# Performance work log

Hardware: AMD Instinct MI355X
Metric: run time of the kernel (lower is better)

The kernel has to match this reference:

```python
import jax, jax.numpy as jnp
import numpy as np

D_HEAD = 128
WINDOW = 512
SCALE = D_HEAD ** -0.5

def setup_inputs() -> dict:
    key = jax.random.key(0)
    kq, kk, kv = jax.random.split(key, 3)
    shape = (4, 16, 2048, D_HEAD)  # [B, H, T, d_head]
    q = jax.random.normal(kq, shape, dtype=jnp.float32)
    k = jax.random.normal(kk, shape, dtype=jnp.float32)
    v = jax.random.normal(kv, shape, dtype=jnp.float32)
    return {"q": q, "k": k, "v": v}

def reference(q, k, v):
    # Sliding-window causal attention (BaseAttention._sliding_window_attention).
    T = q.shape[2]
    scores = jnp.einsum('bhqd,bhkd->bhqk', q, k) * SCALE  # [B,H,T,T]
    i = jnp.arange(T)
    causal = i[None, :] <= i[:, None]                      # j <= i
    in_window = (i[:, None] - i[None, :]) < WINDOW         # i - j < window
    mask = causal & in_window
    scores = jnp.where(mask, scores, -jnp.inf)
    attn = jax.nn.softmax(scores.astype(jnp.float32), axis=-1).astype(v.dtype)
    return jnp.einsum('bhqk,bhkd->bhqd', attn, v)
```

## Files before the change

### kernel.cpp

```cpp
#include <hip/hip_runtime.h>

#define T_SEQ   2048
#define DH      128
#define WINDOW  512
#define BM      128
#define BN      64
#define NT      32
#define TILE_US 16384
#define SCALE_F 0.08838834764831845f

typedef unsigned short ushort_t;
typedef __attribute__((ext_vector_type(8))) unsigned short ushort8;
typedef __attribute__((ext_vector_type(4))) unsigned short ushort4v;
typedef __attribute__((ext_vector_type(4))) float float4v;
typedef __attribute__((ext_vector_type(8))) __bf16 bf16x8;

union U8 { ushort8 us; bf16x8 bf; };

__device__ __forceinline__ unsigned short f2bf(float f) {
  union { float f; unsigned u; } x; x.f = f;
  unsigned r = x.u + 0x7FFFu + ((x.u >> 16) & 1u);
  return (unsigned short)(r >> 16);
}

__device__ __forceinline__ void async16(const ushort_t* g, ushort_t* l) {
  __builtin_amdgcn_global_load_lds(
      (const __attribute__((address_space(1))) unsigned int*)g,
      (__attribute__((address_space(3))) unsigned int*)l, 16, 0, 0);
}

__global__ __launch_bounds__(256)
void pack_kv(const float* __restrict__ kg, const float* __restrict__ vg,
             ushort_t* __restrict__ ws)
{
  const int tile = blockIdx.x;
  const int tid  = threadIdx.x;
  const size_t src = (size_t)tile * (BN * DH);
  const float* kb = kg + src;
  const float* vb = vg + src;
  ushort_t* wk = ws + (size_t)tile * TILE_US;
  ushort_t* wv = wk + 8192;

#pragma unroll
  for (int rep = 0; rep < 4; ++rep) {
    const int b   = rep * 256 + tid;
    const int key = b >> 4;
    const int c8  = b & 15;
    const float* s = kb + key * DH + c8 * 8;
    float4v a = *(const float4v*)s;
    float4v c = *(const float4v*)(s + 4);
    ushort8 h;
    h[0]=f2bf(a[0]); h[1]=f2bf(a[1]); h[2]=f2bf(a[2]); h[3]=f2bf(a[3]);
    h[4]=f2bf(c[0]); h[5]=f2bf(c[1]); h[6]=f2bf(c[2]); h[7]=f2bf(c[3]);
    *(ushort8*)(wk + key * DH + ((c8 ^ (key & 7)) << 3)) = h;
  }

  const int cb  = tid >> 3;
  const int rb0 = tid & 7;
#pragma unroll
  for (int it = 0; it < 2; ++it) {
    const int rb = rb0 + it * 8;
    const float* s = vb + (size_t)(rb * 4) * DH + cb * 4;
    float4v r0 = *(const float4v*)(s);
    float4v r1 = *(const float4v*)(s + DH);
    float4v r2 = *(const float4v*)(s + 2 * DH);
    float4v r3 = *(const float4v*)(s + 3 * DH);
#pragma unroll
    for (int c = 0; c < 4; ++c) {
      const int d = cb * 4 + c;
      ushort4v h;
      h[0]=f2bf(r0[c]); h[1]=f2bf(r1[c]); h[2]=f2bf(r2[c]); h[3]=f2bf(r3[c]);
      *(ushort4v*)(wv + d * BN + (((rb >> 1) ^ (d & 7)) << 3) + (rb & 1) * 4) = h;
    }
  }
}

#define PP 72

__global__ __launch_bounds__(512)
void swa_fwd(const float* __restrict__ qg, const ushort_t* __restrict__ ws,
             float* __restrict__ og)
{
  __shared__ ushort_t lds[TILE_US + 8 * 16 * PP];
  ushort_t* ldsK  = lds;
  ushort_t* ldsVt = lds + 8192;
  ushort_t* ldsP  = lds + TILE_US;

  const int qt   = blockIdx.x;
  const int bh   = blockIdx.y;
  const int tid  = threadIdx.x;
  const int wv   = tid >> 6;
  const int lane = tid & 63;
  const int quad = lane >> 4;
  const int ln16 = lane & 15;
  const int l7   = ln16 & 7;

  const size_t base = (size_t)bh * (T_SEQ * DH);
  const float* qb = qg + base;
  float*       ob = og + base;
  const ushort_t* wsb = ws + (size_t)bh * NT * TILE_US;

  const int i0w = qt * BM + wv * 16;

  bf16x8 qf[4];
  {
    const float* qrow = qb + (size_t)(i0w + ln16) * DH + quad * 8;
#pragma unroll
    for (int ks = 0; ks < 4; ++ks) {
      float4v a = *(const float4v*)(qrow + ks * 32);
      float4v b = *(const float4v*)(qrow + ks * 32 + 4);
      U8 u;
      u.us[0]=f2bf(a[0]*SCALE_F); u.us[1]=f2bf(a[1]*SCALE_F);
      u.us[2]=f2bf(a[2]*SCALE_F); u.us[3]=f2bf(a[3]*SCALE_F);
      u.us[4]=f2bf(b[0]*SCALE_F); u.us[5]=f2bf(b[1]*SCALE_F);
      u.us[6]=f2bf(b[2]*SCALE_F); u.us[7]=f2bf(b[3]*SCALE_F);
      qf[ks] = u.bf;
    }
  }

  float4v Oacc[8];
#pragma unroll
  for (int n = 0; n < 8; ++n) Oacc[n] = (float4v)(0.0f);
  float m_i[4] = {-1e30f, -1e30f, -1e30f, -1e30f};
  float l_i[4] = {0.f, 0.f, 0.f, 0.f};

  const int lo  = qt * BM - (WINDOW - 1);
  const int kt0 = (lo > 0) ? (lo >> 6) : 0;
  const int kt1 = (qt * BM + BM - 1) >> 6;

  for (int kt = kt0; kt <= kt1; ++kt) {
    {
      const ushort_t* wt = wsb + (size_t)kt * TILE_US;
#pragma unroll
      for (int rd = 0; rd < 4; ++rd) {
        const int off = (rd * 512 + tid) * 8;
        async16(wt + off, lds + off);
      }
    }
    __syncthreads();

    const int j0 = kt * BN;
    const bool wave_active = (j0 <= i0w + 15) && (i0w - j0 - 63 < WINDOW);
    if (wave_active) {
      float4v sv[4];
#pragma unroll
      for (int nt = 0; nt < 4; ++nt) {
        float4v acc = (float4v)(0.0f);
        const ushort_t* kp = ldsK + (nt * 16 + ln16) * DH;
#pragma unroll
        for (int ks = 0; ks < 4; ++ks) {
          U8 b; b.us = *(const ushort8*)(kp + (((ks * 4 + quad) ^ l7) << 3));
          acc = __builtin_amdgcn_mfma_f32_16x16x32_bf16(qf[ks], b.bf, acc, 0, 0, 0);
        }
        sv[nt] = acc;
      }

      const bool need_mask = (j0 + 63 > i0w) || ((i0w + 15) - j0 >= WINDOW);
      if (need_mask) {
#pragma unroll
        for (int nt = 0; nt < 4; ++nt) {
          const int j = j0 + nt * 16 + ln16;
#pragma unroll
          for (int r = 0; r < 4; ++r) {
            const int i = i0w + quad * 4 + r;
            const bool ok = (j <= i) && ((i - j) < WINDOW);
            sv[nt][r] = ok ? sv[nt][r] : -1e30f;
          }
        }
      }

      float alpha[4];
#pragma unroll
      for (int r = 0; r < 4; ++r) {
        float mt = fmaxf(fmaxf(sv[0][r], sv[1][r]), fmaxf(sv[2][r], sv[3][r]));
        mt = fmaxf(mt, __shfl_xor(mt, 1));
        mt = fmaxf(mt, __shfl_xor(mt, 2));
        mt = fmaxf(mt, __shfl_xor(mt, 4));
        mt = fmaxf(mt, __shfl_xor(mt, 8));
        const float mn = fmaxf(m_i[r], mt);
        alpha[r] = __expf(m_i[r] - mn);
        m_i[r] = mn;
      }

      ushort_t* pb = ldsP + wv * (16 * PP);
#pragma unroll
      for (int r = 0; r < 4; ++r) {
        float ps = 0.f;
#pragma unroll
        for (int nt = 0; nt < 4; ++nt) {
          const float p = __expf(sv[nt][r] - m_i[r]);
          ps += p;
          pb[(quad * 4 + r) * PP + nt * 16 + ln16] = f2bf(p);
        }
        l_i[r] = l_i[r] * alpha[r] + ps;
#pragma unroll
        for (int n = 0; n < 8; ++n) Oacc[n][r] *= alpha[r];
      }

#pragma unroll
      for (int ks = 0; ks < 2; ++ks) {
        U8 a; a.us = *(const ushort8*)(pb + ln16 * PP + ks * 32 + quad * 8);
#pragma unroll
        for (int n = 0; n < 8; ++n) {
          const ushort_t* vp = ldsVt + (n * 16 + ln16) * BN;
          U8 b; b.us = *(const ushort8*)(vp + (((ks * 4 + quad) ^ l7) << 3));
          Oacc[n] = __builtin_amdgcn_mfma_f32_16x16x32_bf16(a.bf, b.bf, Oacc[n], 0, 0, 0);
        }
      }
    }
    __syncthreads();
  }

  float linv[4];
#pragma unroll
  for (int r = 0; r < 4; ++r) {
    float s = l_i[r];
    s += __shfl_xor(s, 1);
    s += __shfl_xor(s, 2);
    s += __shfl_xor(s, 4);
    s += __shfl_xor(s, 8);
    linv[r] = 1.0f / s;
  }
  float* orow = ob + (size_t)(i0w + quad * 4) * DH + ln16;
#pragma unroll
  for (int r = 0; r < 4; ++r) {
#pragma unroll
    for (int n = 0; n < 8; ++n) {
      orow[(size_t)r * DH + n * 16] = Oacc[n][r] * linv[r];
    }
  }
}

extern "C" void kernel_launch(void* const* d_in, const int* in_sizes, int n_in,
                              void* d_out, int out_size, void* d_ws, size_t ws_size,
                              hipStream_t stream) {
  const float* q = (const float*)d_in[0];
  const float* k = (const float*)d_in[1];
  const float* v = (const float*)d_in[2];
  float* o = (float*)d_out;
  const int bh_count = in_sizes[0] / (T_SEQ * DH);
  ushort_t* ws = (ushort_t*)d_ws;

  pack_kv<<<dim3(bh_count * NT), 256, 0, stream>>>(k, v, ws);
  swa_fwd<<<dim3(T_SEQ / BM, bh_count), 512, 0, stream>>>(q, ws, o);
}
```

Measured before the change: 283.2 us.

## Switch attention to 32x32 MFMA with transposed scores and register-resident P

```diff
diff --git a/kernel.cpp b/kernel.cpp
--- a/kernel.cpp
+++ b/kernel.cpp
@@ -7,18 +7,20 @@
 #define BN      64
 #define NT      32
 #define TILE_US 16384
-#define SCALE_F 0.08838834764831845f
+#define SCALE_LOG2E 0.12751744250f
 
 typedef unsigned short ushort_t;
 typedef __attribute__((ext_vector_type(8))) unsigned short ushort8;
 typedef __attribute__((ext_vector_type(4))) unsigned short ushort4v;
 typedef __attribute__((ext_vector_type(4))) float float4v;
+typedef __attribute__((ext_vector_type(16))) float float16v;
 typedef __attribute__((ext_vector_type(8))) __bf16 bf16x8;
 
-union U8 { ushort8 us; bf16x8 bf; };
+union U8 { ushort8 us; bf16x8 bf; unsigned u[4]; };
+union FU { float f; unsigned u; };
 
 __device__ __forceinline__ unsigned short f2bf(float f) {
-  union { float f; unsigned u; } x; x.f = f;
+  FU x; x.f = f;
   unsigned r = x.u + 0x7FFFu + ((x.u >> 16) & 1u);
   return (unsigned short)(r >> 16);
 }
@@ -33,13 +35,12 @@
 void pack_kv(const float* __restrict__ kg, const float* __restrict__ vg,
              ushort_t* __restrict__ ws)
 {
+  __shared__ __align__(16) ushort_t sb[TILE_US];
   const int tile = blockIdx.x;
   const int tid  = threadIdx.x;
   const size_t src = (size_t)tile * (BN * DH);
   const float* kb = kg + src;
   const float* vb = vg + src;
-  ushort_t* wk = ws + (size_t)tile * TILE_US;
-  ushort_t* wv = wk + 8192;
 
 #pragma unroll
   for (int rep = 0; rep < 4; ++rep) {
@@ -49,184 +50,190 @@
     const float* s = kb + key * DH + c8 * 8;
     float4v a = *(const float4v*)s;
     float4v c = *(const float4v*)(s + 4);
-    ushort8 h;
-    h[0]=f2bf(a[0]); h[1]=f2bf(a[1]); h[2]=f2bf(a[2]); h[3]=f2bf(a[3]);
-    h[4]=f2bf(c[0]); h[5]=f2bf(c[1]); h[6]=f2bf(c[2]); h[7]=f2bf(c[3]);
-    *(ushort8*)(wk + key * DH + ((c8 ^ (key & 7)) << 3)) = h;
-  }
-
-  const int cb  = tid >> 3;
-  const int rb0 = tid & 7;
-#pragma unroll
-  for (int it = 0; it < 2; ++it) {
-    const int rb = rb0 + it * 8;
-    const float* s = vb + (size_t)(rb * 4) * DH + cb * 4;
-    float4v r0 = *(const float4v*)(s);
-    float4v r1 = *(const float4v*)(s + DH);
-    float4v r2 = *(const float4v*)(s + 2 * DH);
-    float4v r3 = *(const float4v*)(s + 3 * DH);
-#pragma unroll
-    for (int c = 0; c < 4; ++c) {
-      const int d = cb * 4 + c;
-      ushort4v h;
-      h[0]=f2bf(r0[c]); h[1]=f2bf(r1[c]); h[2]=f2bf(r2[c]); h[3]=f2bf(r3[c]);
-      *(ushort4v*)(wv + d * BN + (((rb >> 1) ^ (d & 7)) << 3) + (rb & 1) * 4) = h;
-    }
-  }
-}
-
-#define PP 72
-
-__global__ __launch_bounds__(512)
+    U8 h;
+    h.us[0]=f2bf(a[0]); h.us[1]=f2bf(a[1]); h.us[2]=f2bf(a[2]); h.us[3]=f2bf(a[3]);
+    h.us[4]=f2bf(c[0]); h.us[5]=f2bf(c[1]); h.us[6]=f2bf(c[2]); h.us[7]=f2bf(c[3]);
+    *(ushort8*)(sb + key * DH + ((c8 ^ (key & 7)) << 3)) = h.us;
+  }
+
+  {
+    const int cb  = tid >> 3;
+    const int rb0 = tid & 7;
+#pragma unroll
+    for (int it = 0; it < 2; ++it) {
+      const int rb = rb0 + it * 8;
+      const float* s = vb + (size_t)(rb * 4) * DH + cb * 4;
+      float4v r0 = *(const float4v*)(s);
+      float4v r1 = *(const float4v*)(s + DH);
+      float4v r2 = *(const float4v*)(s + 2 * DH);
+      float4v r3 = *(const float4v*)(s + 3 * DH);
+      const int B    = (rb & 1) | ((rb >> 2) << 1);
+      const int off4 = ((rb >> 1) & 1) << 2;
+#pragma unroll
+      for (int c = 0; c < 4; ++c) {
+        const int d = cb * 4 + c;
+        ushort4v h;
+        h[0]=f2bf(r0[c]); h[1]=f2bf(r1[c]); h[2]=f2bf(r2[c]); h[3]=f2bf(r3[c]);
+        *(ushort4v*)(sb + 8192 + d * BN + ((B ^ (d & 7)) << 3) + off4) = h;
+      }
+    }
+  }
+  __syncthreads();
+
+  ushort_t* wt = ws + (size_t)tile * TILE_US;
+#pragma unroll
+  for (int rep = 0; rep < 8; ++rep) {
+    const int off = (rep * 256 + tid) * 8;
+    *(ushort8*)(wt + off) = *(const ushort8*)(sb + off);
+  }
+}
+
+__global__ __launch_bounds__(256, 3)
 void swa_fwd(const float* __restrict__ qg, const ushort_t* __restrict__ ws,
              float* __restrict__ og)
 {
-  __shared__ ushort_t lds[TILE_US + 8 * 16 * PP];
-  ushort_t* ldsK  = lds;
-  ushort_t* ldsVt = lds + 8192;
-  ushort_t* ldsP  = lds + TILE_US;
-
-  const int qt   = blockIdx.x;
+  __shared__ __align__(16) ushort_t lds[TILE_US];
+
+  const int qt   = (gridDim.x - 1) - blockIdx.x;
   const int bh   = blockIdx.y;
   const int tid  = threadIdx.x;
   const int wv   = tid >> 6;
   const int lane = tid & 63;
-  const int quad = lane >> 4;
-  const int ln16 = lane & 15;
-  const int l7   = ln16 & 7;
+  const int l32  = lane & 31;
+  const int half = lane >> 5;
+  const int l7   = l32 & 7;
 
   const size_t base = (size_t)bh * (T_SEQ * DH);
   const float* qb = qg + base;
   float*       ob = og + base;
   const ushort_t* wsb = ws + (size_t)bh * NT * TILE_US;
 
-  const int i0w = qt * BM + wv * 16;
-
-  bf16x8 qf[4];
+  const int i0w = qt * BM + wv * 32;
+  const int iq  = i0w + l32;
+
+  bf16x8 qf[8];
   {
-    const float* qrow = qb + (size_t)(i0w + ln16) * DH + quad * 8;
-#pragma unroll
-    for (int ks = 0; ks < 4; ++ks) {
-      float4v a = *(const float4v*)(qrow + ks * 32);
-      float4v b = *(const float4v*)(qrow + ks * 32 + 4);
+    const float* qrow = qb + (size_t)iq * DH + half * 8;
+#pragma unroll
+    for (int ks = 0; ks < 8; ++ks) {
+      float4v a = *(const float4v*)(qrow + ks * 16);
+      float4v b = *(const float4v*)(qrow + ks * 16 + 4);
       U8 u;
-      u.us[0]=f2bf(a[0]*SCALE_F); u.us[1]=f2bf(a[1]*SCALE_F);
-      u.us[2]=f2bf(a[2]*SCALE_F); u.us[3]=f2bf(a[3]*SCALE_F);
-      u.us[4]=f2bf(b[0]*SCALE_F); u.us[5]=f2bf(b[1]*SCALE_F);
-      u.us[6]=f2bf(b[2]*SCALE_F); u.us[7]=f2bf(b[3]*SCALE_F);
+      u.us[0]=f2bf(a[0]*SCALE_LOG2E); u.us[1]=f2bf(a[1]*SCALE_LOG2E);
+      u.us[2]=f2bf(a[2]*SCALE_LOG2E); u.us[3]=f2bf(a[3]*SCALE_LOG2E);
+      u.us[4]=f2bf(b[0]*SCALE_LOG2E); u.us[5]=f2bf(b[1]*SCALE_LOG2E);
+      u.us[6]=f2bf(b[2]*SCALE_LOG2E); u.us[7]=f2bf(b[3]*SCALE_LOG2E);
       qf[ks] = u.bf;
     }
   }
 
-  float4v Oacc[8];
-#pragma unroll
-  for (int n = 0; n < 8; ++n) Oacc[n] = (float4v)(0.0f);
-  float m_i[4] = {-1e30f, -1e30f, -1e30f, -1e30f};
-  float l_i[4] = {0.f, 0.f, 0.f, 0.f};
+  float16v O[4];
+#pragma unroll
+  for (int dc = 0; dc < 4; ++dc) O[dc] = (float16v)(0.0f);
+  float m = -1e30f, l = 0.f;
 
   const int lo  = qt * BM - (WINDOW - 1);
   const int kt0 = (lo > 0) ? (lo >> 6) : 0;
-  const int kt1 = (qt * BM + BM - 1) >> 6;
+  const int kt1 = 2 * qt + 1;
 
   for (int kt = kt0; kt <= kt1; ++kt) {
     {
       const ushort_t* wt = wsb + (size_t)kt * TILE_US;
 #pragma unroll
-      for (int rd = 0; rd < 4; ++rd) {
-        const int off = (rd * 512 + tid) * 8;
+      for (int rd = 0; rd < 8; ++rd) {
+        const int off = (rd * 256 + tid) * 8;
         async16(wt + off, lds + off);
       }
     }
     __syncthreads();
 
     const int j0 = kt * BN;
-    const bool wave_active = (j0 <= i0w + 15) && (i0w - j0 - 63 < WINDOW);
-    if (wave_active) {
-      float4v sv[4];
-#pragma unroll
-      for (int nt = 0; nt < 4; ++nt) {
-        float4v acc = (float4v)(0.0f);
-        const ushort_t* kp = ldsK + (nt * 16 + ln16) * DH;
-#pragma unroll
-        for (int ks = 0; ks < 4; ++ks) {
-          U8 b; b.us = *(const ushort8*)(kp + (((ks * 4 + quad) ^ l7) << 3));
-          acc = __builtin_amdgcn_mfma_f32_16x16x32_bf16(qf[ks], b.bf, acc, 0, 0, 0);
-        }
-        sv[nt] = acc;
-      }
-
-      const bool need_mask = (j0 + 63 > i0w) || ((i0w + 15) - j0 >= WINDOW);
-      if (need_mask) {
-#pragma unroll
-        for (int nt = 0; nt < 4; ++nt) {
-          const int j = j0 + nt * 16 + ln16;
-#pragma unroll
-          for (int r = 0; r < 4; ++r) {
-            const int i = i0w + quad * 4 + r;
-            const bool ok = (j <= i) && ((i - j) < WINDOW);
-            sv[nt][r] = ok ? sv[nt][r] : -1e30f;
+    const bool active = (j0 <= i0w + 31) && (i0w - j0 - 63 < WINDOW);
+    if (active) {
+      float16v sv[2];
+#pragma unroll
+      for (int c = 0; c < 2; ++c) {
+        float16v acc = (float16v)(0.0f);
+        const ushort_t* krow = lds + (c * 32 + l32) * DH;
+#pragma unroll
+        for (int ks = 0; ks < 8; ++ks) {
+          U8 a; a.us = *(const ushort8*)(krow + (((2 * ks + half) ^ l7) << 3));
+          acc = __builtin_amdgcn_mfma_f32_32x32x16_bf16(a.bf, qf[ks], acc, 0, 0, 0);
+        }
+        sv[c] = acc;
+      }
+
+      const bool full = (j0 + 63 <= i0w) && ((i0w + 31) - j0 < WINDOW);
+      if (!full) {
+#pragma unroll
+        for (int c = 0; c < 2; ++c) {
+#pragma unroll
+          for (int r = 0; r < 16; ++r) {
+            const int j = j0 + c * 32 + (r & 3) + 8 * (r >> 2) + 4 * half;
+            const bool ok = (j <= iq) && ((iq - j) < WINDOW);
+            sv[c][r] = ok ? sv[c][r] : -1e30f;
           }
         }
       }
 
-      float alpha[4];
-#pragma unroll
-      for (int r = 0; r < 4; ++r) {
-        float mt = fmaxf(fmaxf(sv[0][r], sv[1][r]), fmaxf(sv[2][r], sv[3][r]));
-        mt = fmaxf(mt, __shfl_xor(mt, 1));
-        mt = fmaxf(mt, __shfl_xor(mt, 2));
-        mt = fmaxf(mt, __shfl_xor(mt, 4));
-        mt = fmaxf(mt, __shfl_xor(mt, 8));
-        const float mn = fmaxf(m_i[r], mt);
-        alpha[r] = __expf(m_i[r] - mn);
-        m_i[r] = mn;
-      }
-
-      ushort_t* pb = ldsP + wv * (16 * PP);
-#pragma unroll
-      for (int r = 0; r < 4; ++r) {
-        float ps = 0.f;
-#pragma unroll
-        for (int nt = 0; nt < 4; ++nt) {
-          const float p = __expf(sv[nt][r] - m_i[r]);
-          ps += p;
-          pb[(quad * 4 + r) * PP + nt * 16 + ln16] = f2bf(p);
-        }
-        l_i[r] = l_i[r] * alpha[r] + ps;
-#pragma unroll
-        for (int n = 0; n < 8; ++n) Oacc[n][r] *= alpha[r];
-      }
-
-#pragma unroll
-      for (int ks = 0; ks < 2; ++ks) {
-        U8 a; a.us = *(const ushort8*)(pb + ln16 * PP + ks * 32 + quad * 8);
-#pragma unroll
-        for (int n = 0; n < 8; ++n) {
-          const ushort_t* vp = ldsVt + (n * 16 + ln16) * BN;
-          U8 b; b.us = *(const ushort8*)(vp + (((ks * 4 + quad) ^ l7) << 3));
-          Oacc[n] = __builtin_amdgcn_mfma_f32_16x16x32_bf16(a.bf, b.bf, Oacc[n], 0, 0, 0);
+      float mt = sv[0][0];
+#pragma unroll
+      for (int r = 1; r < 16; ++r) mt = fmaxf(mt, sv[0][r]);
+#pragma unroll
+      for (int r = 0; r < 16; ++r) mt = fmaxf(mt, sv[1][r]);
+      mt = fmaxf(mt, __shfl_xor(mt, 32));
+      const float mn = fmaxf(m, mt);
+      const float alpha = __builtin_amdgcn_exp2f(m - mn);
+      m = mn;
+
+      float ps = 0.f;
+      unsigned pk[2][8];
+#pragma unroll
+      for (int c = 0; c < 2; ++c) {
+#pragma unroll
+        for (int rg = 0; rg < 8; ++rg) {
+          FU p0, p1;
+          p0.f = __builtin_amdgcn_exp2f(sv[c][2 * rg]     - m);
+          p1.f = __builtin_amdgcn_exp2f(sv[c][2 * rg + 1] - m);
+          p0.u &= 0xFFFF0000u; p1.u &= 0xFFFF0000u;
+          ps += p0.f + p1.f;
+          pk[c][rg] = (p0.u >> 16) | p1.u;
+        }
+      }
+      l = l * alpha + ps;
+#pragma unroll
+      for (int dc = 0; dc < 4; ++dc)
+#pragma unroll
+        for (int r = 0; r < 16; ++r) O[dc][r] *= alpha;
+
+#pragma unroll
+      for (int s = 0; s < 4; ++s) {
+        const int c = s >> 1, o = (s & 1) * 4;
+        U8 b;
+        b.u[0] = pk[c][o]; b.u[1] = pk[c][o + 1];
+        b.u[2] = pk[c][o + 2]; b.u[3] = pk[c][o + 3];
+        const int blk = ((2 * s + half) ^ l7) << 3;
+#pragma unroll
+        for (int dc = 0; dc < 4; ++dc) {
+          U8 a; a.us = *(const ushort8*)(lds + 8192 + (dc * 32 + l32) * BN + blk);
+          O[dc] = __builtin_amdgcn_mfma_f32_32x32x16_bf16(a.bf, b.bf, O[dc], 0, 0, 0);
         }
       }
     }
     __syncthreads();
   }
 
-  float linv[4];
-#pragma unroll
-  for (int r = 0; r < 4; ++r) {
-    float s = l_i[r];
-    s += __shfl_xor(s, 1);
-    s += __shfl_xor(s, 2);
-    s += __shfl_xor(s, 4);
-    s += __shfl_xor(s, 8);
-    linv[r] = 1.0f / s;
-  }
-  float* orow = ob + (size_t)(i0w + quad * 4) * DH + ln16;
-#pragma unroll
-  for (int r = 0; r < 4; ++r) {
-#pragma unroll
-    for (int n = 0; n < 8; ++n) {
-      orow[(size_t)r * DH + n * 16] = Oacc[n][r] * linv[r];
+  l += __shfl_xor(l, 32);
+  const float linv = 1.0f / l;
+  float* orow = ob + (size_t)iq * DH;
+#pragma unroll
+  for (int dc = 0; dc < 4; ++dc) {
+#pragma unroll
+    for (int g = 0; g < 4; ++g) {
+      float4v o4;
+      o4[0] = O[dc][g * 4 + 0] * linv; o4[1] = O[dc][g * 4 + 1] * linv;
+      o4[2] = O[dc][g * 4 + 2] * linv; o4[3] = O[dc][g * 4 + 3] * linv;
+      *(float4v*)(orow + dc * 32 + g * 8 + half * 4) = o4;
     }
   }
 }
@@ -242,5 +249,5 @@
   ushort_t* ws = (ushort_t*)d_ws;
 
   pack_kv<<<dim3(bh_count * NT), 256, 0, stream>>>(k, v, ws);
-  swa_fwd<<<dim3(T_SEQ / BM, bh_count), 512, 0, stream>>>(q, ws, o);
-}
+  swa_fwd<<<dim3(T_SEQ / BM, bh_count), 256, 0, stream>>>(q, ws, o);
+}
```

Result: no change. 280.1 us (-1.1%).
